# Kernel optimization log

Measured on AMD Instinct MI355X. Metric: run time of the kernel, lower is better.

The kernel has to match this reference:

```python
import jax, jax.numpy as jnp
import numpy as np

N, F_IN, F_OUT, H = 4096, 128, 64, 8
NEG_SLOPE = 0.2

def leaky_relu(x):
    return jnp.where(x >= 0, x, NEG_SLOPE * x)

def setup_inputs() -> dict:
    key = jax.random.key(0)
    k = jax.random.split(key, 6)
    x = jax.random.normal(k[0], (N, F_IN), dtype=jnp.float32)
    conn = jax.random.uniform(k[1], (N, N)) < 0.1
    conn = conn | jnp.eye(N, dtype=bool)
    topology = jnp.where(conn, 0.0, -1e9).astype(jnp.float32)
    proj = jax.random.normal(k[2], (H, F_IN, F_OUT), dtype=jnp.float32) * (1.0 / np.sqrt(F_IN))
    score_src = jax.random.normal(k[3], (H, F_OUT), dtype=jnp.float32) * (1.0 / np.sqrt(F_OUT))
    score_dst = jax.random.normal(k[4], (H, F_OUT), dtype=jnp.float32) * (1.0 / np.sqrt(F_OUT))
    skip_w = jax.random.normal(k[5], (H * F_OUT, F_IN), dtype=jnp.float32) * (1.0 / np.sqrt(F_IN))
    return {"x": x, "topology": topology, "proj": proj,
            "score_src": score_src, "score_dst": score_dst, "skip_w": skip_w}

def reference(x, topology, proj, score_src, score_dst, skip_w):
    # dropout is identity at inference time
    # projected node features: [H, N, F_OUT]
    h = jnp.einsum('ni,hio->hno', x, proj)
    # additive attention scores (GAT): [H, N, 1] + [H, 1, N] -> [H, N, N]
    s_src = jnp.einsum('hno,ho->hn', h, score_src)
    s_dst = jnp.einsum('hno,ho->hn', h, score_dst)
    scores = leaky_relu(s_src[:, :, None] + s_dst[:, None, :])
    attn = jax.nn.softmax(scores + topology[None, :, :], axis=-1)  # [H, N, N]
    # aggregate neighbors, then transpose heads to [N, H, F_OUT]
    out = jnp.einsum('hij,hjo->iho', attn, h)
    # skip connection (F_OUT != F_IN -> projected skip)
    out = out + (x @ skip_w.T).reshape(N, H, F_OUT)
    # mean over heads (concat_heads=False), then LeakyReLU activation
    out = leaky_relu(jnp.mean(out, axis=1))  # [N, F_OUT]
    return out
```

## Files before the change

kernel.cpp:

```cpp
#include <hip/hip_runtime.h>
#include <hip/hip_bf16.h>

#define NN 4096
#define FIN 128
#define FOUT 64
#define NH 8
#define KS 8
#define KRANGE 512
#define QT 128

typedef float f32x4 __attribute__((ext_vector_type(4)));
typedef __bf16 bf16x8 __attribute__((ext_vector_type(8)));
typedef unsigned long long u64;

__global__ __launch_bounds__(256) void wc_kernel(
    const float* __restrict__ proj, const float* __restrict__ score_src,
    const float* __restrict__ score_dst, const float* __restrict__ skip_w,
    float* __restrict__ Wc) {
    int idx = blockIdx.x * 256 + threadIdx.x;
    if (idx >= FIN * 80) return;
    int i = idx / 80, c = idx % 80;
    float v = 0.f;
    if (c < 16) {
        int h = c & 7;
        const float* w = (c < 8 ? score_src : score_dst) + h * FOUT;
        const float* p = proj + (size_t)h * FIN * FOUT + (size_t)i * FOUT;
        for (int f = 0; f < FOUT; ++f) v += p[f] * w[f];
    } else {
        int f = c - 16;
        for (int h = 0; h < NH; ++h) v += skip_w[(size_t)(h * FOUT + f) * FIN + i];
        v *= 0.125f;
    }
    Wc[i * 80 + c] = v;
}

__global__ __launch_bounds__(256) void scores_kernel(
    const float* __restrict__ x, const float* __restrict__ Wc,
    float* __restrict__ skipm, unsigned* __restrict__ EF, float2* __restrict__ C12,
    __hip_bfloat16* __restrict__ xb_) {
    __shared__ float wcs[FIN][80];
    __shared__ float xs[32][FIN + 5];
    const int n0 = blockIdx.x * 32;
    const int tid = threadIdx.x;
    for (int i = tid; i < FIN * 80 / 4; i += 256)
        ((float4*)&wcs[0][0])[i] = ((const float4*)Wc)[i];
    const float4* xsrc = (const float4*)(x + (size_t)n0 * FIN);
    for (int i = tid; i < 32 * FIN / 4; i += 256) {
        int r = i >> 5, c4 = i & 31;
        *(float4*)&xs[r][c4 * 4] = xsrc[i];
    }
    __syncthreads();
    const int r = tid & 31;
    const int g = tid >> 5;
    const int f0 = g * 8;
    const int c0 = g * 2;
    float acc[8];
    float sa0 = 0.f, sa1 = 0.f;
#pragma unroll
    for (int j = 0; j < 8; ++j) acc[j] = 0.f;
#pragma unroll 4
    for (int i = 0; i < FIN; ++i) {
        float xv = xs[r][i];
        float4 p0 = *(float4*)&wcs[i][16 + f0];
        float4 p1 = *(float4*)&wcs[i][16 + f0 + 4];
        float2 q0 = *(float2*)&wcs[i][c0];
        acc[0] += xv * p0.x; acc[1] += xv * p0.y; acc[2] += xv * p0.z; acc[3] += xv * p0.w;
        acc[4] += xv * p1.x; acc[5] += xv * p1.y; acc[6] += xv * p1.z; acc[7] += xv * p1.w;
        sa0 += xv * q0.x; sa1 += xv * q0.y;
    }
    int n = n0 + r;
#pragma unroll
    for (int j = 0; j < 8; ++j) skipm[(size_t)n * FOUT + f0 + j] = acc[j];
    if (c0 < 8) {
        C12[c0 * NN + n] = make_float2(expf(sa0), expf(0.2f * sa0));
        C12[(c0 + 1) * NN + n] = make_float2(expf(sa1), expf(0.2f * sa1));
    } else {
        __hip_bfloat16 e0 = __float2bfloat16(expf(sa0)), f0b = __float2bfloat16(expf(0.2f * sa0));
        __hip_bfloat16 e1 = __float2bfloat16(expf(sa1)), f1b = __float2bfloat16(expf(0.2f * sa1));
        EF[(c0 - 8) * NN + n] = ((unsigned)*(unsigned short*)&f0b << 16) | (unsigned)*(unsigned short*)&e0;
        EF[(c0 - 7) * NN + n] = ((unsigned)*(unsigned short*)&f1b << 16) | (unsigned)*(unsigned short*)&e1;
    }
    {
        int row = tid >> 3, col0 = (tid & 7) * 16;
        const float* src = &xs[row][col0];
        bf16x8 b0, b1;
#pragma unroll
        for (int j = 0; j < 8; ++j) { b0[j] = (__bf16)src[j]; b1[j] = (__bf16)src[8 + j]; }
        __bf16* dst = (__bf16*)xb_ + (size_t)(n0 + row) * FIN + col0;
        *(bf16x8*)dst = b0;
        *(bf16x8*)(dst + 8) = b1;
    }
}

__global__ __launch_bounds__(256) void mask_kernel(
    const float* __restrict__ topo, u64* __restrict__ mb) {
    const int w = blockIdx.x * 4 + (threadIdx.x >> 6);
    const int lane = threadIdx.x & 63;
    size_t base = (size_t)w * 32;
    for (int it = 0; it < 32; ++it) {
        size_t u = base + it;
        float t = topo[u * 64 + lane];
        u64 b = __ballot(t > -0.5e9f);
        if (lane == 0) mb[u] = b;
    }
}

__global__ __launch_bounds__(256) void vt_kernel(
    const float* __restrict__ proj, const __hip_bfloat16* __restrict__ xb_,
    __hip_bfloat16* __restrict__ Vt_) {
    __shared__ __bf16 pT[FOUT][FIN + 8];
    const int tid = threadIdx.x;
    const int h = blockIdx.x >> 6;
    const int ng = blockIdx.x & 63;
    const __bf16* xb = (const __bf16*)xb_;
    __bf16* Vt = (__bf16*)Vt_;
    for (int idx = tid; idx < FIN * FOUT; idx += 256) {
        int i = idx >> 6, f = idx & 63;
        pT[f][i] = (__bf16)proj[(size_t)h * FIN * FOUT + idx];
    }
    __syncthreads();
    const int wave = tid >> 6, lane = tid & 63, q = lane >> 4, li = lane & 15;
    const int nb = ng * 64 + wave * 16;
    f32x4 acc[4];
#pragma unroll
    for (int n = 0; n < 4; ++n) acc[n] = (f32x4){0.f, 0.f, 0.f, 0.f};
#pragma unroll
    for (int kt = 0; kt < 4; ++kt) {
        bf16x8 bfrag = *(const bf16x8*)(xb + (size_t)(nb + li) * FIN + kt * 32 + q * 8);
#pragma unroll
        for (int ft = 0; ft < 4; ++ft) {
            bf16x8 afrag = *(const bf16x8*)&pT[ft * 16 + li][kt * 32 + q * 8];
            acc[ft] = __builtin_amdgcn_mfma_f32_16x16x32_bf16(afrag, bfrag, acc[ft], 0, 0, 0);
        }
    }
#pragma unroll
    for (int ft = 0; ft < 4; ++ft)
#pragma unroll
        for (int reg = 0; reg < 4; ++reg)
            Vt[((size_t)h * FOUT + ft * 16 + q * 4 + reg) * NN + nb + li] = (__bf16)acc[ft][reg];
}

__global__ __launch_bounds__(512, 2) void attn_kernel(
    const u64* __restrict__ maskbits, const __hip_bfloat16* __restrict__ Vt_,
    const unsigned* __restrict__ EFg, const float2* __restrict__ C12g,
    __hip_bfloat16* __restrict__ accP, float* __restrict__ rsP) {
    __shared__ __bf16 vS[2][2][64][64];
    __shared__ u64 maskS[QT][9];
    __shared__ unsigned EFs[NH * KRANGE];
    const int tid = threadIdx.x;
    const int w = tid >> 6, lane = tid & 63, q = lane >> 4, li = lane & 15;
    const int qt = blockIdx.x >> 3, ks = blockIdx.x & 7;
    const int row0 = qt * QT;
    const int kb0 = ks * KRANGE;

    const int fg = lane >> 3, k8 = lane & 7;
    const int swz = ((k8 + fg) & 7) * 8;
    const __bf16* VtB = (const __bf16*)Vt_;

    auto stage = [&](int gg) {
        int h = gg >> 2, T = gg & 3;
        const __bf16* gsrc = VtB + (size_t)h * (FOUT * NN)
                             + (size_t)(w * 8 + fg) * NN + kb0 + T * 128;
        char* lb0 = (char*)&vS[gg & 1][0][w * 8][0];
        char* lb1 = (char*)&vS[gg & 1][1][w * 8][0];
        __builtin_amdgcn_global_load_lds(
            (const __attribute__((address_space(1))) void*)(gsrc + swz),
            (__attribute__((address_space(3))) void*)lb0, 16, 0, 0);
        __builtin_amdgcn_global_load_lds(
            (const __attribute__((address_space(1))) void*)(gsrc + 64 + swz),
            (__attribute__((address_space(3))) void*)lb1, 16, 0, 0);
    };

    stage(0);
    for (int i = tid; i < 1024; i += 512) {
        int r = i >> 3, wd = i & 7;
        maskS[r][wd] = maskbits[(size_t)(row0 + r) * 64 + ks * 8 + wd];
    }
    for (int i = tid; i < 1024; i += 512) {
        int h = i >> 7, k4 = (i & 127) * 4;
        *(uint4*)&EFs[h * KRANGE + k4] = *(const uint4*)&EFg[(size_t)h * NN + kb0 + k4];
    }
    __syncthreads();

#pragma unroll 1
    for (int h = 0; h < NH; ++h) {
        float2 c12 = C12g[(size_t)h * NN + row0 + w * 16 + li];
        const float C1 = c12.x, C2 = c12.y;
        float rs = 0.f;
        f32x4 acc[4];
#pragma unroll
        for (int n = 0; n < 4; ++n) acc[n] = (f32x4){0.f, 0.f, 0.f, 0.f};

#pragma unroll
        for (int T = 0; T < 4; ++T) {
            int gg = h * 4 + T;
            if (gg < 31) stage(gg + 1);
#pragma unroll
            for (int s = 0; s < 2; ++s) {
                u64 mw = maskS[w * 16 + li][T * 2 + s];
                unsigned mlo = (unsigned)(mw >> (q * 8)) & 0xffu;
                unsigned mhi = (unsigned)((mw >> 32) >> (q * 8)) & 0xffu;
                const unsigned* efp = &EFs[h * KRANGE + T * 128 + s * 64];
                uint4 ea = *(const uint4*)&efp[q * 8];
                uint4 eb = *(const uint4*)&efp[q * 8 + 4];
                uint4 ec = *(const uint4*)&efp[32 + q * 8];
                uint4 ed = *(const uint4*)&efp[32 + q * 8 + 4];
                unsigned ew[16] = {ea.x, ea.y, ea.z, ea.w, eb.x, eb.y, eb.z, eb.w,
                                   ec.x, ec.y, ec.z, ec.w, ed.x, ed.y, ed.z, ed.w};
                bf16x8 pf[2];
#pragma unroll
                for (int c = 0; c < 2; ++c) {
                    unsigned mm = c ? mhi : mlo;
#pragma unroll
                    for (int j = 0; j < 8; ++j) {
                        unsigned e = ew[c * 8 + j];
                        float E = __uint_as_float(e << 16);
                        float F = __uint_as_float(e & 0xffff0000u);
                        float pv = fmaxf(C1 * E, C2 * F);
                        pv = ((mm >> j) & 1u) ? pv : 0.f;
                        rs += pv;
                        pf[c][j] = (__bf16)pv;
                    }
                }
#pragma unroll
                for (int c = 0; c < 2; ++c)
#pragma unroll
                    for (int n = 0; n < 4; ++n) {
                        int slot = ((c * 4 + q) - li) & 7;
                        bf16x8 vf = *(const bf16x8*)&vS[gg & 1][s][n * 16 + li][slot * 8];
                        acc[n] = __builtin_amdgcn_mfma_f32_16x16x32_bf16(pf[c], vf, acc[n], 0, 0, 0);
                    }
            }
            __syncthreads();
        }

        rs += __shfl_xor(rs, 16);
        rs += __shfl_xor(rs, 32);
        if (q == 0) rsP[(size_t)(ks * NH + h) * NN + row0 + w * 16 + li] = rs;
        __hip_bfloat16* ap = accP + ((size_t)(ks * NH + h) * NN + row0 + w * 16) * 64;
#pragma unroll
        for (int n = 0; n < 4; ++n)
#pragma unroll
            for (int reg = 0; reg < 4; ++reg)
                ap[(q * 4 + reg) * 64 + n * 16 + li] = __float2bfloat16(acc[n][reg]);
    }
}

__global__ __launch_bounds__(256) void combine_kernel(
    const __hip_bfloat16* __restrict__ accP, const float* __restrict__ rsP,
    float* __restrict__ out) {
    int idx = blockIdx.x * 256 + threadIdx.x;
    int row = idx >> 6, f = idx & 63;
    float s = 0.f;
#pragma unroll 1
    for (int h = 0; h < NH; ++h) {
        float a = 0.f, r = 0.f;
#pragma unroll
        for (int k = 0; k < KS; ++k) {
            a += __bfloat162float(accP[((size_t)(k * NH + h) * NN + row) * 64 + f]);
            r += rsP[(size_t)(k * NH + h) * NN + row];
        }
        s += a / r;
    }
    float v = s * 0.125f + out[idx];
    out[idx] = fmaxf(v, 0.2f * v);
}

extern "C" void kernel_launch(void* const* d_in, const int* in_sizes, int n_in,
                              void* d_out, int out_size, void* d_ws, size_t ws_size,
                              hipStream_t stream) {
    (void)in_sizes; (void)n_in; (void)out_size; (void)ws_size;
    const float* x         = (const float*)d_in[0];
    const float* topology  = (const float*)d_in[1];
    const float* proj      = (const float*)d_in[2];
    const float* score_src = (const float*)d_in[3];
    const float* score_dst = (const float*)d_in[4];
    const float* skip_w    = (const float*)d_in[5];
    float* out = (float*)d_out;

    char* ws = (char*)d_ws;
    __hip_bfloat16* xb = (__hip_bfloat16*)ws;
    __hip_bfloat16* Vt = (__hip_bfloat16*)(ws + 1048576);
    unsigned* EF  = (unsigned*)(ws + 5242880);
    float2* C12   = (float2*)(ws + 5373952);
    float* Wc     = (float*)(ws + 5636096);
    u64* maskbits = (u64*)(ws + 5677056);
    float* rsP    = (float*)(ws + 7774208);
    __hip_bfloat16* accP = (__hip_bfloat16*)(ws + 8822784);
    float* skipm = out;

    wc_kernel<<<40, 256, 0, stream>>>(proj, score_src, score_dst, skip_w, Wc);
    scores_kernel<<<128, 256, 0, stream>>>(x, Wc, skipm, EF, C12, xb);
    mask_kernel<<<2048, 256, 0, stream>>>(topology, maskbits);
    vt_kernel<<<512, 256, 0, stream>>>(proj, xb, Vt);
    attn_kernel<<<256, 512, 0, stream>>>(maskbits, Vt, EF, C12, accP, rsP);
    combine_kernel<<<1024, 256, 0, stream>>>(accP, rsP, out);
}
```

Before: 203.3 us.

## Restructure attention kernel to one head per wave with direct global loads

The attention kernel now assigns each wave one head and covers 64 query rows with four row tiles, so each loaded V fragment is reused across four row tiles from registers. The LDS double-buffered staging of V and the LDS copy of the EF scores are gone, along with the per-tile barriers, and the grid doubles by halving the query tile to 64. The scores kernel is also split finer (16 rows per block, twice the blocks), and the mask kernel loop is unrolled. The trade-off is more register pressure from 16 accumulators per wave and V being read straight from global memory/L2 without shared staging.

```diff
diff --git a/kernel.cpp b/kernel.cpp
--- a/kernel.cpp
+++ b/kernel.cpp
@@ -6,8 +6,7 @@
 #define FOUT 64
 #define NH 8
 #define KS 8
-#define KRANGE 512
-#define QT 128
+#define QT 64
 
 typedef float f32x4 __attribute__((ext_vector_type(4)));
 typedef __bf16 bf16x8 __attribute__((ext_vector_type(8)));
@@ -39,56 +38,48 @@
     float* __restrict__ skipm, unsigned* __restrict__ EF, float2* __restrict__ C12,
     __hip_bfloat16* __restrict__ xb_) {
     __shared__ float wcs[FIN][80];
-    __shared__ float xs[32][FIN + 5];
-    const int n0 = blockIdx.x * 32;
+    __shared__ float xs[16][FIN + 5];
+    const int n0 = blockIdx.x * 16;
     const int tid = threadIdx.x;
     for (int i = tid; i < FIN * 80 / 4; i += 256)
         ((float4*)&wcs[0][0])[i] = ((const float4*)Wc)[i];
     const float4* xsrc = (const float4*)(x + (size_t)n0 * FIN);
-    for (int i = tid; i < 32 * FIN / 4; i += 256) {
+    for (int i = tid; i < 16 * FIN / 4; i += 256) {
         int r = i >> 5, c4 = i & 31;
         *(float4*)&xs[r][c4 * 4] = xsrc[i];
     }
     __syncthreads();
-    const int r = tid & 31;
-    const int g = tid >> 5;
-    const int f0 = g * 8;
-    const int c0 = g * 2;
-    float acc[8];
-    float sa0 = 0.f, sa1 = 0.f;
-#pragma unroll
-    for (int j = 0; j < 8; ++j) acc[j] = 0.f;
+    const int r = tid & 15;
+    const int g = tid >> 4;
+    float acc[4];
+    float sa = 0.f;
+#pragma unroll
+    for (int j = 0; j < 4; ++j) acc[j] = 0.f;
 #pragma unroll 4
     for (int i = 0; i < FIN; ++i) {
         float xv = xs[r][i];
-        float4 p0 = *(float4*)&wcs[i][16 + f0];
-        float4 p1 = *(float4*)&wcs[i][16 + f0 + 4];
-        float2 q0 = *(float2*)&wcs[i][c0];
-        acc[0] += xv * p0.x; acc[1] += xv * p0.y; acc[2] += xv * p0.z; acc[3] += xv * p0.w;
-        acc[4] += xv * p1.x; acc[5] += xv * p1.y; acc[6] += xv * p1.z; acc[7] += xv * p1.w;
-        sa0 += xv * q0.x; sa1 += xv * q0.y;
+        float4 p = *(float4*)&wcs[i][16 + g * 4];
+        float qv = wcs[i][g];
+        acc[0] += xv * p.x; acc[1] += xv * p.y; acc[2] += xv * p.z; acc[3] += xv * p.w;
+        sa += xv * qv;
     }
     int n = n0 + r;
 #pragma unroll
-    for (int j = 0; j < 8; ++j) skipm[(size_t)n * FOUT + f0 + j] = acc[j];
-    if (c0 < 8) {
-        C12[c0 * NN + n] = make_float2(expf(sa0), expf(0.2f * sa0));
-        C12[(c0 + 1) * NN + n] = make_float2(expf(sa1), expf(0.2f * sa1));
+    for (int j = 0; j < 4; ++j) skipm[(size_t)n * FOUT + g * 4 + j] = acc[j];
+    if (g < 8) {
+        C12[g * NN + n] = make_float2(expf(sa), expf(0.2f * sa));
     } else {
-        __hip_bfloat16 e0 = __float2bfloat16(expf(sa0)), f0b = __float2bfloat16(expf(0.2f * sa0));
-        __hip_bfloat16 e1 = __float2bfloat16(expf(sa1)), f1b = __float2bfloat16(expf(0.2f * sa1));
-        EF[(c0 - 8) * NN + n] = ((unsigned)*(unsigned short*)&f0b << 16) | (unsigned)*(unsigned short*)&e0;
-        EF[(c0 - 7) * NN + n] = ((unsigned)*(unsigned short*)&f1b << 16) | (unsigned)*(unsigned short*)&e1;
+        __hip_bfloat16 e0 = __float2bfloat16(expf(sa));
+        __hip_bfloat16 f0 = __float2bfloat16(expf(0.2f * sa));
+        EF[(g - 8) * NN + n] = ((unsigned)*(unsigned short*)&f0 << 16) | (unsigned)*(unsigned short*)&e0;
     }
     {
-        int row = tid >> 3, col0 = (tid & 7) * 16;
+        int row = tid >> 4, col0 = (tid & 15) * 8;
         const float* src = &xs[row][col0];
-        bf16x8 b0, b1;
-#pragma unroll
-        for (int j = 0; j < 8; ++j) { b0[j] = (__bf16)src[j]; b1[j] = (__bf16)src[8 + j]; }
-        __bf16* dst = (__bf16*)xb_ + (size_t)(n0 + row) * FIN + col0;
-        *(bf16x8*)dst = b0;
-        *(bf16x8*)(dst + 8) = b1;
+        bf16x8 b0;
+#pragma unroll
+        for (int j = 0; j < 8; ++j) b0[j] = (__bf16)src[j];
+        *(bf16x8*)((__bf16*)xb_ + (size_t)(n0 + row) * FIN + col0) = b0;
     }
 }
 
@@ -97,6 +88,7 @@
     const int w = blockIdx.x * 4 + (threadIdx.x >> 6);
     const int lane = threadIdx.x & 63;
     size_t base = (size_t)w * 32;
+#pragma unroll 4
     for (int it = 0; it < 32; ++it) {
         size_t u = base + it;
         float t = topo[u * 64 + lane];
@@ -140,109 +132,88 @@
             Vt[((size_t)h * FOUT + ft * 16 + q * 4 + reg) * NN + nb + li] = (__bf16)acc[ft][reg];
 }
 
-__global__ __launch_bounds__(512, 2) void attn_kernel(
+__attribute__((amdgpu_waves_per_eu(4, 4)))
+__global__ __launch_bounds__(512) void attn_kernel(
     const u64* __restrict__ maskbits, const __hip_bfloat16* __restrict__ Vt_,
     const unsigned* __restrict__ EFg, const float2* __restrict__ C12g,
     __hip_bfloat16* __restrict__ accP, float* __restrict__ rsP) {
-    __shared__ __bf16 vS[2][2][64][64];
     __shared__ u64 maskS[QT][9];
-    __shared__ unsigned EFs[NH * KRANGE];
     const int tid = threadIdx.x;
-    const int w = tid >> 6, lane = tid & 63, q = lane >> 4, li = lane & 15;
+    const int h = tid >> 6;
+    const int lane = tid & 63, q = lane >> 4, li = lane & 15;
     const int qt = blockIdx.x >> 3, ks = blockIdx.x & 7;
     const int row0 = qt * QT;
-    const int kb0 = ks * KRANGE;
-
-    const int fg = lane >> 3, k8 = lane & 7;
-    const int swz = ((k8 + fg) & 7) * 8;
-    const __bf16* VtB = (const __bf16*)Vt_;
-
-    auto stage = [&](int gg) {
-        int h = gg >> 2, T = gg & 3;
-        const __bf16* gsrc = VtB + (size_t)h * (FOUT * NN)
-                             + (size_t)(w * 8 + fg) * NN + kb0 + T * 128;
-        char* lb0 = (char*)&vS[gg & 1][0][w * 8][0];
-        char* lb1 = (char*)&vS[gg & 1][1][w * 8][0];
-        __builtin_amdgcn_global_load_lds(
-            (const __attribute__((address_space(1))) void*)(gsrc + swz),
-            (__attribute__((address_space(3))) void*)lb0, 16, 0, 0);
-        __builtin_amdgcn_global_load_lds(
-            (const __attribute__((address_space(1))) void*)(gsrc + 64 + swz),
-            (__attribute__((address_space(3))) void*)lb1, 16, 0, 0);
-    };
-
-    stage(0);
-    for (int i = tid; i < 1024; i += 512) {
-        int r = i >> 3, wd = i & 7;
+    const int kb0 = ks * 512;
+
+    {
+        int r = tid >> 3, wd = tid & 7;
         maskS[r][wd] = maskbits[(size_t)(row0 + r) * 64 + ks * 8 + wd];
     }
-    for (int i = tid; i < 1024; i += 512) {
-        int h = i >> 7, k4 = (i & 127) * 4;
-        *(uint4*)&EFs[h * KRANGE + k4] = *(const uint4*)&EFg[(size_t)h * NN + kb0 + k4];
-    }
     __syncthreads();
 
-#pragma unroll 1
-    for (int h = 0; h < NH; ++h) {
-        float2 c12 = C12g[(size_t)h * NN + row0 + w * 16 + li];
-        const float C1 = c12.x, C2 = c12.y;
-        float rs = 0.f;
-        f32x4 acc[4];
-#pragma unroll
-        for (int n = 0; n < 4; ++n) acc[n] = (f32x4){0.f, 0.f, 0.f, 0.f};
-
-#pragma unroll
-        for (int T = 0; T < 4; ++T) {
-            int gg = h * 4 + T;
-            if (gg < 31) stage(gg + 1);
-#pragma unroll
-            for (int s = 0; s < 2; ++s) {
-                u64 mw = maskS[w * 16 + li][T * 2 + s];
-                unsigned mlo = (unsigned)(mw >> (q * 8)) & 0xffu;
-                unsigned mhi = (unsigned)((mw >> 32) >> (q * 8)) & 0xffu;
-                const unsigned* efp = &EFs[h * KRANGE + T * 128 + s * 64];
-                uint4 ea = *(const uint4*)&efp[q * 8];
-                uint4 eb = *(const uint4*)&efp[q * 8 + 4];
-                uint4 ec = *(const uint4*)&efp[32 + q * 8];
-                uint4 ed = *(const uint4*)&efp[32 + q * 8 + 4];
-                unsigned ew[16] = {ea.x, ea.y, ea.z, ea.w, eb.x, eb.y, eb.z, eb.w,
-                                   ec.x, ec.y, ec.z, ec.w, ed.x, ed.y, ed.z, ed.w};
-                bf16x8 pf[2];
-#pragma unroll
-                for (int c = 0; c < 2; ++c) {
-                    unsigned mm = c ? mhi : mlo;
-#pragma unroll
-                    for (int j = 0; j < 8; ++j) {
-                        unsigned e = ew[c * 8 + j];
-                        float E = __uint_as_float(e << 16);
-                        float F = __uint_as_float(e & 0xffff0000u);
-                        float pv = fmaxf(C1 * E, C2 * F);
-                        pv = ((mm >> j) & 1u) ? pv : 0.f;
-                        rs += pv;
-                        pf[c][j] = (__bf16)pv;
-                    }
-                }
-#pragma unroll
-                for (int c = 0; c < 2; ++c)
-#pragma unroll
-                    for (int n = 0; n < 4; ++n) {
-                        int slot = ((c * 4 + q) - li) & 7;
-                        bf16x8 vf = *(const bf16x8*)&vS[gg & 1][s][n * 16 + li][slot * 8];
-                        acc[n] = __builtin_amdgcn_mfma_f32_16x16x32_bf16(pf[c], vf, acc[n], 0, 0, 0);
-                    }
+    const __bf16* vb = (const __bf16*)Vt_ + (size_t)h * (FOUT * NN) + kb0;
+    const unsigned* efb = EFg + (size_t)h * NN + kb0;
+    float C1[4], C2[4];
+#pragma unroll
+    for (int rt = 0; rt < 4; ++rt) {
+        float2 c = C12g[(size_t)h * NN + row0 + rt * 16 + li];
+        C1[rt] = c.x; C2[rt] = c.y;
+    }
+
+    f32x4 acc[4][4];
+#pragma unroll
+    for (int rt = 0; rt < 4; ++rt)
+#pragma unroll
+        for (int n = 0; n < 4; ++n) acc[rt][n] = (f32x4){0.f, 0.f, 0.f, 0.f};
+    float rs[4] = {0.f, 0.f, 0.f, 0.f};
+
+#pragma unroll 2
+    for (int kt = 0; kt < 16; ++kt) {
+        const unsigned* ep = efb + kt * 32 + q * 8;
+        uint4 ea = *(const uint4*)ep;
+        uint4 eb = *(const uint4*)(ep + 4);
+        bf16x8 vf[4];
+#pragma unroll
+        for (int n = 0; n < 4; ++n)
+            vf[n] = *(const bf16x8*)(vb + (size_t)(n * 16 + li) * NN + kt * 32 + q * 8);
+        unsigned ew[8] = {ea.x, ea.y, ea.z, ea.w, eb.x, eb.y, eb.z, eb.w};
+        float E[8], F[8];
+#pragma unroll
+        for (int j = 0; j < 8; ++j) {
+            E[j] = __uint_as_float(ew[j] << 16);
+            F[j] = __uint_as_float(ew[j] & 0xffff0000u);
+        }
+#pragma unroll
+        for (int rt = 0; rt < 4; ++rt) {
+            u64 mw = maskS[rt * 16 + li][kt >> 1];
+            unsigned grp = (unsigned)(mw >> ((kt & 1) * 32));
+            unsigned mm = (grp >> (q * 8)) & 0xffu;
+            bf16x8 pf;
+#pragma unroll
+            for (int j = 0; j < 8; ++j) {
+                float pv = fmaxf(C1[rt] * E[j], C2[rt] * F[j]);
+                pv = ((mm >> j) & 1u) ? pv : 0.f;
+                rs[rt] += pv;
+                pf[j] = (__bf16)pv;
             }
-            __syncthreads();
-        }
-
-        rs += __shfl_xor(rs, 16);
-        rs += __shfl_xor(rs, 32);
-        if (q == 0) rsP[(size_t)(ks * NH + h) * NN + row0 + w * 16 + li] = rs;
-        __hip_bfloat16* ap = accP + ((size_t)(ks * NH + h) * NN + row0 + w * 16) * 64;
+#pragma unroll
+            for (int n = 0; n < 4; ++n)
+                acc[rt][n] = __builtin_amdgcn_mfma_f32_16x16x32_bf16(pf, vf[n], acc[rt][n], 0, 0, 0);
+        }
+    }
+
+#pragma unroll
+    for (int rt = 0; rt < 4; ++rt) {
+        float r = rs[rt];
+        r += __shfl_xor(r, 16);
+        r += __shfl_xor(r, 32);
+        if (q == 0) rsP[(size_t)(ks * NH + h) * NN + row0 + rt * 16 + li] = r;
+        __hip_bfloat16* ap = accP + ((size_t)(ks * NH + h) * NN + row0 + rt * 16) * 64;
 #pragma unroll
         for (int n = 0; n < 4; ++n)
 #pragma unroll
             for (int reg = 0; reg < 4; ++reg)
-                ap[(q * 4 + reg) * 64 + n * 16 + li] = __float2bfloat16(acc[n][reg]);
+                ap[(q * 4 + reg) * 64 + n * 16 + li] = __float2bfloat16(acc[rt][n][reg]);
     }
 }
 
@@ -290,9 +261,9 @@
     float* skipm = out;
 
     wc_kernel<<<40, 256, 0, stream>>>(proj, score_src, score_dst, skip_w, Wc);
-    scores_kernel<<<128, 256, 0, stream>>>(x, Wc, skipm, EF, C12, xb);
+    scores_kernel<<<256, 256, 0, stream>>>(x, Wc, skipm, EF, C12, xb);
     mask_kernel<<<2048, 256, 0, stream>>>(topology, maskbits);
     vt_kernel<<<512, 256, 0, stream>>>(proj, xb, Vt);
-    attn_kernel<<<256, 512, 0, stream>>>(maskbits, Vt, EF, C12, accP, rsP);
+    attn_kernel<<<512, 512, 0, stream>>>(maskbits, Vt, EF, C12, accP, rsP);
     combine_kernel<<<1024, 256, 0, stream>>>(accP, rsP, out);
 }
```

Result: slower. 281.4 us (+38.4%).
